# Kernel optimization log

Hardware: AMD Instinct MI355X
Metric: run time of the kernel (lower is better)

Reference implementation:

```python
import jax, jax.numpy as jnp
import numpy as np

DIM = 768
H = 12
HD = DIM // H
LN_EPS = 1e-5


def setup_inputs() -> dict:
    key = jax.random.key(0)
    ks = jax.random.split(key, 8)
    B, N, C = 64, 197, DIM
    s = 0.02
    return {
        "x": jax.random.normal(ks[0], (B, N, C), jnp.float32),
        "qkv_w": jax.random.normal(ks[1], (C, 3 * C), jnp.float32) * s,
        "qkv_b": jnp.zeros((3 * C,), jnp.float32),
        "proj_w": jax.random.normal(ks[2], (C, C), jnp.float32) * s,
        "proj_b": jnp.zeros((C,), jnp.float32),
        "ht_w": jax.random.normal(ks[3], (HD, C), jnp.float32) * s,
        "ht_b": jnp.zeros((C,), jnp.float32),
        "ln_g": jnp.ones((HD,), jnp.float32),
        "ln_b": jnp.zeros((HD,), jnp.float32),
        "pos_embed": jax.random.normal(ks[4], (1, H, C), jnp.float32) * s,
    }


def reference(x, qkv_w, qkv_b, proj_w, proj_b, ht_w, ht_b, ln_g, ln_b, pos_embed):
    B, N, C = x.shape
    scale = HD ** -0.5
    # head tokens: mean over sequence per head -> [B, H, HD]
    ht = x.reshape(B, N, H, HD).mean(axis=1)
    ht = ht @ ht_w + ht_b                      # [B, H, C]
    ht = ht.reshape(B, H, H, HD)
    mu = ht.mean(axis=-1, keepdims=True)
    var = jnp.mean((ht - mu) ** 2, axis=-1, keepdims=True)
    ht = (ht - mu) * jax.lax.rsqrt(var + LN_EPS) * ln_g + ln_b
    ht = jax.nn.gelu(ht, approximate=False).reshape(B, H, C) + pos_embed
    xc = jnp.concatenate([x, ht], axis=1)      # [B, T=N+H, C]
    T = N + H
    qkv = (xc @ qkv_w + qkv_b).reshape(B, T, 3, H, HD)
    q, k, v = qkv[:, :, 0], qkv[:, :, 1], qkv[:, :, 2]  # [B, T, H, HD]
    attn = jnp.einsum('bqhd,bkhd->bhqk', q, k) * scale
    attn = jax.nn.softmax(attn, axis=-1)
    out = jnp.einsum('bhqk,bkhd->bqhd', attn, v).reshape(B, T, C)
    out = out @ proj_w + proj_b
    cls = out[:, :1] + out[:, N:].mean(axis=1, keepdims=True)
    return jnp.concatenate([cls, out[:, 1:N]], axis=1)
```

## Files before the change

### kernel.cpp

```cpp
#include <hip/hip_runtime.h>
#include <cstdint>
#include <cstddef>

typedef unsigned short u16;
typedef __attribute__((ext_vector_type(8))) __bf16 bf16x8;
typedef __attribute__((ext_vector_type(4))) unsigned short u16x4;
typedef __attribute__((ext_vector_type(8))) unsigned short u16x8;
typedef __attribute__((ext_vector_type(4))) float f32x4;

#define NTOK 197
#define TT   209
#define CDIM 768
#define NH   12
#define HD   64
#define BATCH 64
#define GM (BATCH*TT)
#define VTP 224
#define NQKV 2304

__device__ __forceinline__ float bf2f(u16 u){ return __uint_as_float(((unsigned)u)<<16); }
__device__ __forceinline__ u16 f2bf(float f){
  unsigned x = __float_as_uint(f);
  return (u16)((x + 0x7FFFu + ((x>>16)&1u)) >> 16);
}

__device__ __forceinline__ void gll16(const void* g, void* l){
  __builtin_amdgcn_global_load_lds((const __attribute__((address_space(1))) void*)g,
                                   (__attribute__((address_space(3))) void*)l,
                                   16, 0, 0);
}

__device__ __forceinline__ float wsum64(float v){
  #pragma unroll
  for (int o = 32; o > 0; o >>= 1) v += __shfl_xor(v, o, 64);
  return v;
}

__global__ __launch_bounds__(64) void detect_kernel(const u16* __restrict__ x, int* flag){
  const int lane = threadIdx.x;
  float mx = 0.f;
  #pragma unroll
  for (int i = 0; i < 16; i++) {
    float v = fabsf(bf2f(x[i*64 + lane]));
    if (!(v < 1e30f)) v = 1e30f;
    mx = fmaxf(mx, v);
  }
  #pragma unroll
  for (int o = 32; o; o >>= 1) mx = fmaxf(mx, __shfl_xor(mx, o, 64));
  if (lane == 0) *flag = (mx < 1e5f) ? 1 : 0;
}

struct CA { const void* in[10]; void* out[10]; int n[10]; };
__global__ __launch_bounds__(256) void convert_all_kernel(CA a, const int* __restrict__ flag){
  const int seg = blockIdx.y;
  if (seg == 1 || seg == 3) return;
  const int f = *flag;
  if (seg == 0 && f) return;
  const int n = a.n[seg];
  const int n4 = n >> 2;
  u16* out = (u16*)a.out[seg];
  if (f) {
    const u16x4* in = (const u16x4*)a.in[seg];
    for (int i = blockIdx.x*256 + threadIdx.x; i < n4; i += gridDim.x*256)
      ((u16x4*)out)[i] = in[i];
  } else {
    const f32x4* in = (const f32x4*)a.in[seg];
    for (int i = blockIdx.x*256 + threadIdx.x; i < n4; i += gridDim.x*256){
      f32x4 v = in[i];
      u16x4 o;
      #pragma unroll
      for (int j=0;j<4;j++) o[j] = f2bf(v[j]);
      ((u16x4*)out)[i] = o;
    }
  }
  if (blockIdx.x == 0 && (int)threadIdx.x < (n & 3)) {
    int i = (n4 << 2) + threadIdx.x;
    out[i] = f ? ((const u16*)a.in[seg])[i] : f2bf(((const float*)a.in[seg])[i]);
  }
}

__global__ __launch_bounds__(256) void transpose2_kernel(
    const void* __restrict__ w1, const void* __restrict__ w2,
    u16* __restrict__ o1, u16* __restrict__ o2, const int* __restrict__ flag)
{
  __shared__ u16 lds[64][66];
  const int f = *flag;
  int bid = blockIdx.x;
  const void* in; u16* out; int K, N, tx, ty;
  if (bid < 432) { in = w1; out = o1; K = CDIM; N = NQKV; tx = bid % 36; ty = bid / 36; }
  else { bid -= 432; in = w2; out = o2; K = CDIM; N = CDIM; tx = bid % 12; ty = bid / 12; }
  const int n0 = tx*64, k0 = ty*64;
  const int c = threadIdx.x & 63, r0 = threadIdx.x >> 6;
  #pragma unroll
  for (int i=0;i<16;i++) {
    int r = i*4 + r0;
    size_t idx = (size_t)(k0+r)*N + n0 + c;
    lds[r][c] = f ? ((const u16*)in)[idx] : f2bf(((const float*)in)[idx]);
  }
  __syncthreads();
  #pragma unroll
  for (int i=0;i<16;i++) {
    int r = i*4 + r0;
    out[(size_t)(n0+r)*K + k0 + c] = lds[c][r];
  }
}

__global__ __launch_bounds__(256) void mean_kernel(
    const u16* __restrict__ xc, const void* __restrict__ xr,
    float* __restrict__ mbuf, const int* __restrict__ flag)
{
  const int b = blockIdx.x, s = blockIdx.y;
  const int tid = threadIdx.x;
  const int f = *flag;
  const u16* x = f ? (const u16*)xr : xc;
  const u16* xp = x + (size_t)b*NTOK*CDIM + s*256 + tid;
  float cs = 0.f;
  for (int n = 0; n < NTOK; n++) cs += bf2f(xp[(size_t)n*CDIM]);
  mbuf[(size_t)b*CDIM + s*256 + tid] = cs * (1.0f/(float)NTOK);
}

__global__ __launch_bounds__(256) void htmm_kernel(
    const float* __restrict__ mbuf,
    const u16* __restrict__ htw, const u16* __restrict__ htb,
    const u16* __restrict__ lng, const u16* __restrict__ lnb,
    const u16* __restrict__ pos, u16* __restrict__ ht)
{
  const int b = blockIdx.x, h = blockIdx.y;
  const int tid = threadIdx.x;
  __shared__ float msh[64];
  if (tid < 64) msh[tid] = mbuf[(size_t)b*CDIM + h*HD + tid];
  __syncthreads();

  float v0 = bf2f(htb[tid]), v1 = bf2f(htb[tid+256]), v2 = bf2f(htb[tid+512]);
  for (int d = 0; d < HD; d++) {
    const float md = msh[d];
    const u16* wr = htw + (size_t)d*CDIM;
    v0 += md * bf2f(wr[tid]);
    v1 += md * bf2f(wr[tid+256]);
    v2 += md * bf2f(wr[tid+512]);
  }
  const float gam = bf2f(lng[tid & 63]), bet = bf2f(lnb[tid & 63]);
  float vv[3] = {v0, v1, v2};
  #pragma unroll
  for (int ch = 0; ch < 3; ch++) {
    int c = ch*256 + tid;
    float mu = wsum64(vv[ch]) * (1.0f/(float)HD);
    float dv = vv[ch] - mu;
    float var = wsum64(dv*dv) * (1.0f/(float)HD);
    float y = dv * rsqrtf(var + 1e-5f) * gam + bet;
    float ge = 0.5f * y * (1.0f + erff(y * 0.70710678118654752f));
    float o = ge + bf2f(pos[h*CDIM + c]);
    ht[((size_t)(b*NH + h))*CDIM + c] = f2bf(o);
  }
}

template<int MODE>
__global__ __launch_bounds__(256, 2) void gemm_kernel(
    const u16* __restrict__ A0c, const void* __restrict__ A0r,
    const u16* __restrict__ A1,
    const u16* __restrict__ Bt, const u16* __restrict__ bias,
    u16* __restrict__ qout,
    void* __restrict__ outv, float* __restrict__ csb, const int* __restrict__ flag)
{
  const int tid = threadIdx.x;
  const int lane = tid & 63;
  const int w = tid >> 6;
  const int wm = w >> 1, wn = w & 1;
  const int lr = lane & 15, kg = lane >> 4;

  const int NT = gridDim.x;
  const int nwg = NT * gridDim.y;
  const int orig = blockIdx.y * NT + blockIdx.x;
  const int xcd = orig & 7, sIdx = orig >> 3;
  const int q = nwg >> 3, r = nwg & 7;
  const int wg = ((xcd < r) ? xcd*(q+1) : r*(q+1) + (xcd-r)*q) + sIdx;
  const int tm = wg / NT, tn = wg - tm*NT;

  __shared__ __align__(16) u16 As[5][4096];
  __shared__ __align__(16) u16 Bs[5][4096];

  const int f = *flag;
  const u16* A0 = (MODE == 0) ? (f ? (const u16*)A0r : A0c) : A0c;

  f32x4 acc[4][4];
  #pragma unroll
  for (int i=0;i<4;i++)
    #pragma unroll
    for (int j=0;j<4;j++) acc[i][j] = (f32x4){0.f,0.f,0.f,0.f};

  const u16* garow[2];
  const u16* gbrow[2];
  #pragma unroll
  for (int i=0;i<2;i++){
    int row = (i*4 + w)*16 + (lane >> 2);
    int rr = tm*128 + row; if (rr > GM-1) rr = GM-1;
    if (MODE == 0) {
      int bb = rr / TT; int t = rr - bb*TT;
      garow[i] = (t < NTOK) ? (A0 + (size_t)(bb*NTOK + t)*CDIM)
                            : (A1 + (size_t)(bb*NH + (t - NTOK))*CDIM);
    } else {
      garow[i] = A0 + (size_t)rr*CDIM;
    }
    gbrow[i] = Bt + (size_t)(tn*128 + row)*CDIM;
  }
  const int gseg = (lane & 3) ^ ((lane >> 3) & 3);

#define STAGE(kt_, bf_) do { \
    const int ko_ = (kt_)*32 + gseg*8; \
    gll16(garow[0] + ko_, (void*)&As[bf_][(0*4+w)*512]); \
    gll16(garow[1] + ko_, (void*)&As[bf_][(1*4+w)*512]); \
    gll16(gbrow[0] + ko_, (void*)&Bs[bf_][(0*4+w)*512]); \
    gll16(gbrow[1] + ko_, (void*)&Bs[bf_][(1*4+w)*512]); \
  } while(0)

  STAGE(0, 0);
  STAGE(1, 1);
  STAGE(2, 2);

  const int spA = kg ^ ((lr >> 1) & 3);

  #pragma unroll
  for (int kt = 0; kt < 24; kt++) {
    const int cb = kt % 5;
    if (kt < 21) {
      STAGE(kt+3, (kt+3)%5);
      asm volatile("s_waitcnt vmcnt(12)" ::: "memory");
    } else if (kt == 21) {
      asm volatile("s_waitcnt vmcnt(8)" ::: "memory");
    } else if (kt == 22) {
      asm volatile("s_waitcnt vmcnt(4)" ::: "memory");
    } else {
      asm volatile("s_waitcnt vmcnt(0)" ::: "memory");
    }
    __builtin_amdgcn_s_barrier();

    bf16x8 av[4], bv[4];
    #pragma unroll
    for (int mi=0; mi<4; mi++)
      av[mi] = *(const bf16x8*)&As[cb][(wm*64+mi*16+lr)*32 + spA*8];
    #pragma unroll
    for (int ni=0; ni<4; ni++)
      bv[ni] = *(const bf16x8*)&Bs[cb][(wn*64+ni*16+lr)*32 + spA*8];
    #pragma unroll
    for (int mi=0; mi<4; mi++)
      #pragma unroll
      for (int ni=0; ni<4; ni++)
        acc[mi][ni] = __builtin_amdgcn_mfma_f32_16x16x32_bf16(av[mi], bv[ni], acc[mi][ni], 0,0,0);
  }
#undef STAGE

  #pragma unroll
  for (int mi=0; mi<4; mi++){
    const int rb = tm*128 + wm*64 + mi*16 + kg*4;
    #pragma unroll
    for (int ni=0; ni<4; ni++){
      const int c = tn*128 + wn*64 + ni*16 + lr;
      const float bs = bf2f(bias[c]);
      if (MODE == 0) {
        #pragma unroll
        for (int j=0;j<4;j++){
          int rr = rb + j;
          if (rr < GM) qout[(size_t)rr*NQKV + c] = f2bf(acc[mi][ni][j] + bs);
        }
      } else {
        #pragma unroll
        for (int j=0;j<4;j++){
          int rr = rb + j;
          if (rr < GM) {
            int bb = rr / TT; int t = rr - bb*TT;
            float v = acc[mi][ni][j] + bs;
            if (t >= 1 && t < NTOK) {
              size_t oi = ((size_t)(bb*NTOK + t))*CDIM + c;
              if (f) ((u16*)outv)[oi] = f2bf(v);
              else   ((float*)outv)[oi] = v;
            } else {
              int idx = (t == 0) ? 0 : (t - NTOK + 1);
              csb[((size_t)(bb*13 + idx))*CDIM + c] = v;
            }
          }
        }
      }
    }
  }
}

__global__ __launch_bounds__(256) void vtrans_kernel(
    const u16* __restrict__ qkvo, u16* __restrict__ vb)
{
  __shared__ u16 lds[64][66];
  const int tt0 = blockIdx.x*64;
  const int bh = blockIdx.y;
  const int b = bh / NH, h = bh - b*NH;
  const int c = threadIdx.x & 63, r0 = threadIdx.x >> 6;
  #pragma unroll
  for (int i=0;i<16;i++) {
    int t = tt0 + i*4 + r0;
    u16 v = 0;
    if (t < TT) v = qkvo[(size_t)(b*TT + t)*NQKV + 1536 + h*64 + c];
    lds[i*4+r0][c] = v;
  }
  __syncthreads();
  #pragma unroll
  for (int i=0;i<16;i++) {
    int d = i*4 + r0;
    int t = tt0 + c;
    if (t < VTP) vb[((size_t)(bh)*HD + d)*VTP + t] = lds[c][d];
  }
}

__global__ __launch_bounds__(256) void attn_kernel(
    const u16* __restrict__ qkvo, const u16* __restrict__ vt, u16* __restrict__ ob)
{
  __shared__ __align__(16) u16 Kl[224*72];
  __shared__ __align__(16) u16 P[4][7*16*32];
  const int tid = threadIdx.x;
  const int lane = tid & 63;
  const int w = tid >> 6;
  const int lr = lane & 15, kg = lane >> 4;

  const int bh = blockIdx.x;
  const int b = bh / NH, h = bh - b*NH;

  const u16* qg  = qkvo + (size_t)(b*TT)*NQKV + h*64;
  const u16* kgp = qg + CDIM;
  const u16* vg  = vt + (size_t)bh*HD*VTP;

  for (int s = tid; s < 224*8; s += 256) {
    int kc = s >> 3, seg = s & 7;
    uint4 val = make_uint4(0,0,0,0);
    if (kc < TT) val = *(const uint4*)&kgp[(size_t)kc*NQKV + seg*8];
    *(uint4*)&Kl[kc*72 + seg*8] = val;
  }
  __syncthreads();

  u16* Pw = &P[w][0];
  for (int ck = w; ck < 14; ck += 4) {
    const int q0 = ck*16;
    int qrow = q0 + lr; if (qrow > TT-1) qrow = TT-1;
    const bf16x8 qf0 = *(const bf16x8*)&qg[(size_t)qrow*NQKV + kg*8];
    const bf16x8 qf1 = *(const bf16x8*)&qg[(size_t)qrow*NQKV + 32 + kg*8];

    f32x4 sv[14];
    #pragma unroll
    for (int kt = 0; kt < 14; kt++) {
      bf16x8 kf0 = *(const bf16x8*)&Kl[(kt*16+lr)*72 + kg*8];
      bf16x8 kf1 = *(const bf16x8*)&Kl[(kt*16+lr)*72 + 32 + kg*8];
      f32x4 sa = {0.f,0.f,0.f,0.f};
      sa = __builtin_amdgcn_mfma_f32_16x16x32_bf16(kf0, qf0, sa, 0,0,0);
      sa = __builtin_amdgcn_mfma_f32_16x16x32_bf16(kf1, qf1, sa, 0,0,0);
      sv[kt] = sa;
    }

    float m = -3.0e38f;
    #pragma unroll
    for (int kt = 0; kt < 13; kt++)
      #pragma unroll
      for (int j=0;j<4;j++){ sv[kt][j] *= 0.125f; m = fmaxf(m, sv[kt][j]); }
    #pragma unroll
    for (int j=0;j<4;j++){
      sv[13][j] *= 0.125f;
      if (208 + kg*4 + j < TT) m = fmaxf(m, sv[13][j]);
    }
    m = fmaxf(m, __shfl_xor(m, 16, 64));
    m = fmaxf(m, __shfl_xor(m, 32, 64));

    float ssum = 0.f;
    #pragma unroll
    for (int kt = 0; kt < 13; kt++)
      #pragma unroll
      for (int j=0;j<4;j++){ float e = __expf(sv[kt][j] - m); sv[kt][j] = e; ssum += e; }
    #pragma unroll
    for (int j=0;j<4;j++){
      float e = (208 + kg*4 + j < TT) ? __expf(sv[13][j] - m) : 0.f;
      sv[13][j] = e; ssum += e;
    }
    ssum += __shfl_xor(ssum, 16, 64);
    ssum += __shfl_xor(ssum, 32, 64);
    const float inv = 1.0f / ssum;

    #pragma unroll
    for (int kt = 0; kt < 14; kt++) {
      u16x4 pk;
      #pragma unroll
      for (int j=0;j<4;j++) pk[j] = f2bf(sv[kt][j] * inv);
      *(u16x4*)&Pw[(kt>>1)*512 + lr*32 + (kt&1)*16 + kg*4] = pk;
    }

    f32x4 acc[4];
    #pragma unroll
    for (int dt=0; dt<4; dt++) acc[dt] = (f32x4){0.f,0.f,0.f,0.f};
    #pragma unroll
    for (int ks = 0; ks < 7; ks++) {
      bf16x8 pf = *(const bf16x8*)&Pw[ks*512 + lr*32 + kg*8];
      #pragma unroll
      for (int dt = 0; dt < 4; dt++) {
        bf16x8 vf = *(const bf16x8*)&vg[(dt*16+lr)*VTP + ks*32 + kg*8];
        acc[dt] = __builtin_amdgcn_mfma_f32_16x16x32_bf16(pf, vf, acc[dt], 0,0,0);
      }
    }

    #pragma unroll
    for (int dt = 0; dt < 4; dt++)
      #pragma unroll
      for (int j = 0; j < 4; j++) {
        int tq = q0 + kg*4 + j;
        if (tq < TT)
          ob[((size_t)(b*TT + tq))*CDIM + h*HD + dt*16 + lr] = f2bf(acc[dt][j]);
      }
  }
}

__global__ __launch_bounds__(256) void final2_kernel(
    const float* __restrict__ csb, void* __restrict__ outv, const int* __restrict__ flag)
{
  const int f = *flag;
  int i = blockIdx.x*256 + threadIdx.x;
  if (i >= BATCH*CDIM) return;
  int b = i / CDIM, c = i - b*CDIM;
  const float* p = csb + (size_t)b*13*CDIM + c;
  float s = 0.f;
  #pragma unroll
  for (int j = 1; j <= 12; j++) s += p[(size_t)j*CDIM];
  float v = p[0] + s * (1.0f/12.0f);
  size_t oi = ((size_t)b*NTOK)*CDIM + c;
  if (f) ((u16*)outv)[oi] = f2bf(v);
  else   ((float*)outv)[oi] = v;
}

extern "C" void kernel_launch(void* const* d_in, const int* in_sizes, int n_in,
                              void* d_out, int out_size, void* d_ws, size_t ws_size,
                              hipStream_t stream)
{
  char* ws = (char*)d_ws;
  size_t off = 0;
  auto alloc = [&](size_t bytes)->void* {
    void* p = ws + off; off += (bytes + 255) & ~(size_t)255; return p;
  };

  int* flag = (int*)alloc(256);

  u16* cin[10];
  for (int i = 0; i < 10; i++) cin[i] = (u16*)alloc((size_t)in_sizes[i]*2);

  u16* qkvT  = (u16*)alloc((size_t)3*CDIM*CDIM*2);
  u16* projT = (u16*)alloc((size_t)CDIM*CDIM*2);
  u16* htb_  = (u16*)alloc((size_t)BATCH*NH*CDIM*2);
  float* mbuf = (float*)alloc((size_t)BATCH*CDIM*4);
  u16* qkvo  = (u16*)alloc((size_t)GM*NQKV*2);
  u16* vb    = (u16*)alloc((size_t)BATCH*NH*HD*VTP*2);
  float* csb = (float*)alloc((size_t)BATCH*13*CDIM*4);
  u16* ao    = cin[0];

  detect_kernel<<<1, 64, 0, stream>>>((const u16*)d_in[0], flag);

  CA ca;
  for (int i = 0; i < 10; i++) { ca.in[i] = d_in[i]; ca.out[i] = cin[i]; ca.n[i] = in_sizes[i]; }
  convert_all_kernel<<<dim3(256, 10), 256, 0, stream>>>(ca, flag);

  transpose2_kernel<<<576, 256, 0, stream>>>(d_in[1], d_in[3], qkvT, projT, flag);
  mean_kernel<<<dim3(BATCH, 3), 256, 0, stream>>>(cin[0], d_in[0], mbuf, flag);
  htmm_kernel<<<dim3(BATCH, NH), 256, 0, stream>>>(mbuf, cin[5], cin[6], cin[7], cin[8], cin[9], htb_);
  gemm_kernel<0><<<dim3(NQKV/128, (GM+127)/128), 256, 0, stream>>>(
      cin[0], d_in[0], htb_, qkvT, cin[2], qkvo, nullptr, nullptr, flag);
  vtrans_kernel<<<dim3(4, BATCH*NH), 256, 0, stream>>>(qkvo, vb);
  attn_kernel<<<BATCH*NH, 256, 0, stream>>>(qkvo, vb, ao);
  gemm_kernel<1><<<dim3(CDIM/128, (GM+127)/128), 256, 0, stream>>>(
      ao, nullptr, nullptr, projT, cin[4], nullptr, d_out, csb, flag);
  final2_kernel<<<(BATCH*CDIM+255)/256, 256, 0, stream>>>(csb, d_out, flag);
}
```

Measured before the change: 235.7 us.

## Merge prep kernels into one launch and recompute dtype flag per block

Replaces the detect, convert, transpose, mean and head-token kernels with a single prep kernel whose block ranges handle x conversion, weight transposes and the head-token mean/matmul/LN/GELU. The dtype flag is no longer stored in a buffer: every block recomputes it from the first elements of x. Small parameters such as biases, LN params and pos are read directly in either format instead of being converted first. This cuts launch count and intermediate buffer traffic, at the cost of repeating the detection reads in every block and a less uniform prep kernel.

```diff
diff --git a/kernel.cpp b/kernel.cpp
--- a/kernel.cpp
+++ b/kernel.cpp
@@ -5,7 +5,6 @@
 typedef unsigned short u16;
 typedef __attribute__((ext_vector_type(8))) __bf16 bf16x8;
 typedef __attribute__((ext_vector_type(4))) unsigned short u16x4;
-typedef __attribute__((ext_vector_type(8))) unsigned short u16x8;
 typedef __attribute__((ext_vector_type(4))) float f32x4;
 
 #define NTOK 197
@@ -17,6 +16,7 @@
 #define GM (BATCH*TT)
 #define VTP 224
 #define NQKV 2304
+#define XN (BATCH*NTOK*CDIM)
 
 __device__ __forceinline__ float bf2f(u16 u){ return __uint_as_float(((unsigned)u)<<16); }
 __device__ __forceinline__ u16 f2bf(float f){
@@ -36,8 +36,8 @@
   return v;
 }
 
-__global__ __launch_bounds__(64) void detect_kernel(const u16* __restrict__ x, int* flag){
-  const int lane = threadIdx.x;
+__device__ __forceinline__ int detect_f(const u16* __restrict__ x){
+  const int lane = threadIdx.x & 63;
   float mx = 0.f;
   #pragma unroll
   for (int i = 0; i < 16; i++) {
@@ -47,110 +47,92 @@
   }
   #pragma unroll
   for (int o = 32; o; o >>= 1) mx = fmaxf(mx, __shfl_xor(mx, o, 64));
-  if (lane == 0) *flag = (mx < 1e5f) ? 1 : 0;
-}
-
-struct CA { const void* in[10]; void* out[10]; int n[10]; };
-__global__ __launch_bounds__(256) void convert_all_kernel(CA a, const int* __restrict__ flag){
-  const int seg = blockIdx.y;
-  if (seg == 1 || seg == 3) return;
-  const int f = *flag;
-  if (seg == 0 && f) return;
-  const int n = a.n[seg];
-  const int n4 = n >> 2;
-  u16* out = (u16*)a.out[seg];
-  if (f) {
-    const u16x4* in = (const u16x4*)a.in[seg];
-    for (int i = blockIdx.x*256 + threadIdx.x; i < n4; i += gridDim.x*256)
-      ((u16x4*)out)[i] = in[i];
-  } else {
-    const f32x4* in = (const f32x4*)a.in[seg];
-    for (int i = blockIdx.x*256 + threadIdx.x; i < n4; i += gridDim.x*256){
+  return mx < 1e5f;
+}
+
+__device__ __forceinline__ float ldany(const void* p, size_t i, int f){
+  return f ? bf2f(((const u16*)p)[i]) : ((const float*)p)[i];
+}
+
+__global__ __launch_bounds__(256) void prep_kernel(
+    const void* __restrict__ xr, const void* __restrict__ w1, const void* __restrict__ w2,
+    const void* __restrict__ htw, const void* __restrict__ htb,
+    const void* __restrict__ lng, const void* __restrict__ lnb, const void* __restrict__ pos,
+    u16* __restrict__ xc, u16* __restrict__ o1, u16* __restrict__ o2,
+    u16* __restrict__ ht)
+{
+  const int tid = threadIdx.x;
+  const int f = detect_f((const u16*)xr);
+  const int bid = blockIdx.x;
+  __shared__ u16 lds[64][66];
+  __shared__ float part[4][64];
+  __shared__ float msh[64];
+
+  if (bid < 256) {
+    if (f) return;
+    const f32x4* in = (const f32x4*)xr;
+    const int n4 = XN >> 2;
+    for (int i = bid*256 + tid; i < n4; i += 256*256) {
       f32x4 v = in[i];
       u16x4 o;
       #pragma unroll
       for (int j=0;j<4;j++) o[j] = f2bf(v[j]);
-      ((u16x4*)out)[i] = o;
-    }
-  }
-  if (blockIdx.x == 0 && (int)threadIdx.x < (n & 3)) {
-    int i = (n4 << 2) + threadIdx.x;
-    out[i] = f ? ((const u16*)a.in[seg])[i] : f2bf(((const float*)a.in[seg])[i]);
-  }
-}
-
-__global__ __launch_bounds__(256) void transpose2_kernel(
-    const void* __restrict__ w1, const void* __restrict__ w2,
-    u16* __restrict__ o1, u16* __restrict__ o2, const int* __restrict__ flag)
-{
-  __shared__ u16 lds[64][66];
-  const int f = *flag;
-  int bid = blockIdx.x;
-  const void* in; u16* out; int K, N, tx, ty;
-  if (bid < 432) { in = w1; out = o1; K = CDIM; N = NQKV; tx = bid % 36; ty = bid / 36; }
-  else { bid -= 432; in = w2; out = o2; K = CDIM; N = CDIM; tx = bid % 12; ty = bid / 12; }
-  const int n0 = tx*64, k0 = ty*64;
-  const int c = threadIdx.x & 63, r0 = threadIdx.x >> 6;
-  #pragma unroll
-  for (int i=0;i<16;i++) {
-    int r = i*4 + r0;
-    size_t idx = (size_t)(k0+r)*N + n0 + c;
-    lds[r][c] = f ? ((const u16*)in)[idx] : f2bf(((const float*)in)[idx]);
-  }
+      ((u16x4*)xc)[i] = o;
+    }
+    return;
+  }
+  if (bid < 832) {
+    const void* in; u16* out; int N, tx, ty;
+    if (bid < 688) { int t = bid-256; in = w1; out = o1; N = NQKV; tx = t % 36; ty = t / 36; }
+    else           { int t = bid-688; in = w2; out = o2; N = CDIM; tx = t % 12; ty = t / 12; }
+    const int n0 = tx*64, k0 = ty*64;
+    const int c = tid & 63, r0 = tid >> 6;
+    #pragma unroll
+    for (int i=0;i<16;i++) {
+      int r = i*4 + r0;
+      size_t idx = (size_t)(k0+r)*N + n0 + c;
+      lds[r][c] = f ? ((const u16*)in)[idx] : f2bf(((const float*)in)[idx]);
+    }
+    __syncthreads();
+    #pragma unroll
+    for (int i=0;i<16;i++) {
+      int r = i*4 + r0;
+      out[(size_t)(n0+r)*CDIM + k0 + c] = lds[c][r];
+    }
+    return;
+  }
+
+  const int idx = bid - 832;
+  const int b = idx / NH, h = idx - b*NH;
+  const int c = tid & 63, rg = tid >> 6;
+  float s = 0.f;
+  for (int n = rg; n < NTOK; n += 4)
+    s += ldany(xr, (size_t)(b*NTOK + n)*CDIM + h*HD + c, f);
+  part[rg][c] = s;
   __syncthreads();
-  #pragma unroll
-  for (int i=0;i<16;i++) {
-    int r = i*4 + r0;
-    out[(size_t)(n0+r)*K + k0 + c] = lds[c][r];
-  }
-}
-
-__global__ __launch_bounds__(256) void mean_kernel(
-    const u16* __restrict__ xc, const void* __restrict__ xr,
-    float* __restrict__ mbuf, const int* __restrict__ flag)
-{
-  const int b = blockIdx.x, s = blockIdx.y;
-  const int tid = threadIdx.x;
-  const int f = *flag;
-  const u16* x = f ? (const u16*)xr : xc;
-  const u16* xp = x + (size_t)b*NTOK*CDIM + s*256 + tid;
-  float cs = 0.f;
-  for (int n = 0; n < NTOK; n++) cs += bf2f(xp[(size_t)n*CDIM]);
-  mbuf[(size_t)b*CDIM + s*256 + tid] = cs * (1.0f/(float)NTOK);
-}
-
-__global__ __launch_bounds__(256) void htmm_kernel(
-    const float* __restrict__ mbuf,
-    const u16* __restrict__ htw, const u16* __restrict__ htb,
-    const u16* __restrict__ lng, const u16* __restrict__ lnb,
-    const u16* __restrict__ pos, u16* __restrict__ ht)
-{
-  const int b = blockIdx.x, h = blockIdx.y;
-  const int tid = threadIdx.x;
-  __shared__ float msh[64];
-  if (tid < 64) msh[tid] = mbuf[(size_t)b*CDIM + h*HD + tid];
+  if (tid < 64) msh[tid] = (part[0][tid]+part[1][tid]+part[2][tid]+part[3][tid]) * (1.0f/(float)NTOK);
   __syncthreads();
 
-  float v0 = bf2f(htb[tid]), v1 = bf2f(htb[tid+256]), v2 = bf2f(htb[tid+512]);
+  float v0 = ldany(htb, tid, f), v1 = ldany(htb, tid+256, f), v2 = ldany(htb, tid+512, f);
   for (int d = 0; d < HD; d++) {
     const float md = msh[d];
-    const u16* wr = htw + (size_t)d*CDIM;
-    v0 += md * bf2f(wr[tid]);
-    v1 += md * bf2f(wr[tid+256]);
-    v2 += md * bf2f(wr[tid+512]);
-  }
-  const float gam = bf2f(lng[tid & 63]), bet = bf2f(lnb[tid & 63]);
+    const size_t wr = (size_t)d*CDIM;
+    v0 += md * ldany(htw, wr + tid, f);
+    v1 += md * ldany(htw, wr + tid + 256, f);
+    v2 += md * ldany(htw, wr + tid + 512, f);
+  }
+  const float gam = ldany(lng, tid & 63, f), bet = ldany(lnb, tid & 63, f);
   float vv[3] = {v0, v1, v2};
   #pragma unroll
   for (int ch = 0; ch < 3; ch++) {
-    int c = ch*256 + tid;
+    int cc = ch*256 + tid;
     float mu = wsum64(vv[ch]) * (1.0f/(float)HD);
     float dv = vv[ch] - mu;
     float var = wsum64(dv*dv) * (1.0f/(float)HD);
     float y = dv * rsqrtf(var + 1e-5f) * gam + bet;
     float ge = 0.5f * y * (1.0f + erff(y * 0.70710678118654752f));
-    float o = ge + bf2f(pos[h*CDIM + c]);
-    ht[((size_t)(b*NH + h))*CDIM + c] = f2bf(o);
+    float o = ge + ldany(pos, h*CDIM + cc, f);
+    ht[((size_t)(b*NH + h))*CDIM + cc] = f2bf(o);
   }
 }
 
@@ -158,15 +140,16 @@
 __global__ __launch_bounds__(256, 2) void gemm_kernel(
     const u16* __restrict__ A0c, const void* __restrict__ A0r,
     const u16* __restrict__ A1,
-    const u16* __restrict__ Bt, const u16* __restrict__ bias,
+    const u16* __restrict__ Bt, const void* __restrict__ bias,
     u16* __restrict__ qout,
-    void* __restrict__ outv, float* __restrict__ csb, const int* __restrict__ flag)
+    void* __restrict__ outv, float* __restrict__ csb, const u16* __restrict__ xdet)
 {
   const int tid = threadIdx.x;
   const int lane = tid & 63;
   const int w = tid >> 6;
   const int wm = w >> 1, wn = w & 1;
   const int lr = lane & 15, kg = lane >> 4;
+  const int f = detect_f(xdet);
 
   const int NT = gridDim.x;
   const int nwg = NT * gridDim.y;
@@ -179,7 +162,6 @@
   __shared__ __align__(16) u16 As[5][4096];
   __shared__ __align__(16) u16 Bs[5][4096];
 
-  const int f = *flag;
   const u16* A0 = (MODE == 0) ? (f ? (const u16*)A0r : A0c) : A0c;
 
   f32x4 acc[4][4];
@@ -255,7 +237,7 @@
     #pragma unroll
     for (int ni=0; ni<4; ni++){
       const int c = tn*128 + wn*64 + ni*16 + lr;
-      const float bs = bf2f(bias[c]);
+      const float bs = ldany(bias, c, f);
       if (MODE == 0) {
         #pragma unroll
         for (int j=0;j<4;j++){
@@ -411,9 +393,9 @@
 }
 
 __global__ __launch_bounds__(256) void final2_kernel(
-    const float* __restrict__ csb, void* __restrict__ outv, const int* __restrict__ flag)
-{
-  const int f = *flag;
+    const float* __restrict__ csb, void* __restrict__ outv, const u16* __restrict__ xdet)
+{
+  const int f = detect_f(xdet);
   int i = blockIdx.x*256 + threadIdx.x;
   if (i >= BATCH*CDIM) return;
   int b = i / CDIM, c = i - b*CDIM;
@@ -437,34 +419,25 @@
     void* p = ws + off; off += (bytes + 255) & ~(size_t)255; return p;
   };
 
-  int* flag = (int*)alloc(256);
-
-  u16* cin[10];
-  for (int i = 0; i < 10; i++) cin[i] = (u16*)alloc((size_t)in_sizes[i]*2);
-
+  u16* xconv = (u16*)alloc((size_t)XN*2);
   u16* qkvT  = (u16*)alloc((size_t)3*CDIM*CDIM*2);
   u16* projT = (u16*)alloc((size_t)CDIM*CDIM*2);
   u16* htb_  = (u16*)alloc((size_t)BATCH*NH*CDIM*2);
-  float* mbuf = (float*)alloc((size_t)BATCH*CDIM*4);
   u16* qkvo  = (u16*)alloc((size_t)GM*NQKV*2);
   u16* vb    = (u16*)alloc((size_t)BATCH*NH*HD*VTP*2);
   float* csb = (float*)alloc((size_t)BATCH*13*CDIM*4);
-  u16* ao    = cin[0];
-
-  detect_kernel<<<1, 64, 0, stream>>>((const u16*)d_in[0], flag);
-
-  CA ca;
-  for (int i = 0; i < 10; i++) { ca.in[i] = d_in[i]; ca.out[i] = cin[i]; ca.n[i] = in_sizes[i]; }
-  convert_all_kernel<<<dim3(256, 10), 256, 0, stream>>>(ca, flag);
-
-  transpose2_kernel<<<576, 256, 0, stream>>>(d_in[1], d_in[3], qkvT, projT, flag);
-  mean_kernel<<<dim3(BATCH, 3), 256, 0, stream>>>(cin[0], d_in[0], mbuf, flag);
-  htmm_kernel<<<dim3(BATCH, NH), 256, 0, stream>>>(mbuf, cin[5], cin[6], cin[7], cin[8], cin[9], htb_);
+  u16* ao    = xconv;
+
+  const u16* xdet = (const u16*)d_in[0];
+
+  prep_kernel<<<1600, 256, 0, stream>>>(
+      d_in[0], d_in[1], d_in[3], d_in[5], d_in[6], d_in[7], d_in[8], d_in[9],
+      xconv, qkvT, projT, htb_);
   gemm_kernel<0><<<dim3(NQKV/128, (GM+127)/128), 256, 0, stream>>>(
-      cin[0], d_in[0], htb_, qkvT, cin[2], qkvo, nullptr, nullptr, flag);
+      xconv, d_in[0], htb_, qkvT, d_in[2], qkvo, nullptr, nullptr, xdet);
   vtrans_kernel<<<dim3(4, BATCH*NH), 256, 0, stream>>>(qkvo, vb);
   attn_kernel<<<BATCH*NH, 256, 0, stream>>>(qkvo, vb, ao);
   gemm_kernel<1><<<dim3(CDIM/128, (GM+127)/128), 256, 0, stream>>>(
-      ao, nullptr, nullptr, projT, cin[4], nullptr, d_out, csb, flag);
-  final2_kernel<<<(BATCH*CDIM+255)/256, 256, 0, stream>>>(csb, d_out, flag);
-}
+      ao, nullptr, nullptr, projT, d_in[4], nullptr, d_out, csb, xdet);
+  final2_kernel<<<(BATCH*CDIM+255)/256, 256, 0, stream>>>(csb, d_out, xdet);
+}
```

After: 253.3 us. +7.5%, slower.
